# Performance work log

Measured on AMD Instinct MI355X. Metric: run time of the kernel, lower is better.

The kernel has to match this reference:

```python
import jax, jax.numpy as jnp
import numpy as np

D_MODEL = 1024
NUM_HEADS = 16
D_HEAD = D_MODEL // NUM_HEADS  # 64
LAMBDA_INIT = 0.8
EPS = 1e-5


def setup_inputs() -> dict:
    key = jax.random.key(0)
    ks = jax.random.split(key, 10)
    B, N = 2, 2048
    # Xavier-uniform-ish scale for the projection weights
    def xav(k, shape):
        fan_in, fan_out = shape[0], shape[1]
        lim = np.sqrt(6.0 / (fan_in + fan_out))
        return jax.random.uniform(k, shape, jnp.float32, -lim, lim)
    return {
        "X": jax.random.normal(ks[0], (B, N, D_MODEL), jnp.float32),
        "Wq": xav(ks[1], (D_MODEL, 2 * D_MODEL)),
        "Wk": xav(ks[2], (D_MODEL, 2 * D_MODEL)),
        "Wv": xav(ks[3], (D_MODEL, 2 * D_MODEL)),
        "Wo": xav(ks[4], (2 * D_MODEL, D_MODEL)),
        "lambda_q1": jax.random.normal(ks[5], (NUM_HEADS, D_HEAD), jnp.float32),
        "lambda_k1": jax.random.normal(ks[6], (NUM_HEADS, D_HEAD), jnp.float32),
        "lambda_q2": jax.random.normal(ks[7], (NUM_HEADS, D_HEAD), jnp.float32),
        "lambda_k2": jax.random.normal(ks[8], (NUM_HEADS, D_HEAD), jnp.float32),
        "rms_scale": jnp.ones((2 * D_HEAD,), jnp.float32),
    }


def reference(X, Wq, Wk, Wv, Wo, lambda_q1, lambda_k1, lambda_q2, lambda_k2, rms_scale):
    B, N, _ = X.shape
    H, Dh = NUM_HEADS, D_HEAD
    # projections -> [B, H, N, 2*Dh]
    Q = (X @ Wq).reshape(B, N, H, 2 * Dh).transpose(0, 2, 1, 3)
    K = (X @ Wk).reshape(B, N, H, 2 * Dh).transpose(0, 2, 1, 3)
    V = (X @ Wv).reshape(B, N, H, 2 * Dh).transpose(0, 2, 1, 3)
    Q1, Q2 = Q[..., :Dh], Q[..., Dh:]
    K1, K2 = K[..., :Dh], K[..., Dh:]
    # learned lambda per head
    lam = (jnp.exp(jnp.sum(lambda_q1 * lambda_k1, -1))
           - jnp.exp(jnp.sum(lambda_q2 * lambda_k2, -1))
           + LAMBDA_INIT)  # [H]
    scaling = 1.0 / np.sqrt(Dh)
    causal = jnp.tril(jnp.ones((N, N), bool))  # [N, N]
    neg_inf = jnp.float32(-jnp.inf)
    A1 = jnp.einsum('bhqd,bhkd->bhqk', Q1, K1) * scaling
    A2 = jnp.einsum('bhqd,bhkd->bhqk', Q2, K2) * scaling
    A1 = jnp.where(causal, A1, neg_inf)
    A2 = jnp.where(causal, A2, neg_inf)
    attn = jax.nn.softmax(A1, axis=-1) - lam[None, :, None, None] * jax.nn.softmax(A2, axis=-1)
    O = jnp.einsum('bhqk,bhkd->bhqd', attn, V)  # [B, H, N, 2*Dh]
    # per-(batch,head,pos) RMSNorm over the 2*Dh channel dim
    rms = jnp.sqrt(jnp.mean(O * O, axis=-1, keepdims=True) + EPS)
    O = O / rms * rms_scale
    O = O * (1.0 - LAMBDA_INIT)
    O = O.transpose(0, 2, 1, 3).reshape(B, N, H * 2 * Dh)
    return O @ Wo
```

## Files before the change

### kernel.cpp

```cpp
#include <hip/hip_runtime.h>
#include <hip/hip_bf16.h>

#define DM   1024
#define NH   16
#define DH   64
#define NSEQ 2048
#define NBATCH 2
#define ROWS (NBATCH*NSEQ)
#define QKVN (2*DM)
#define STR3 (3*DM*2)

typedef __attribute__((ext_vector_type(8))) short short8;
typedef __attribute__((ext_vector_type(4))) float f32x4;
typedef __attribute__((ext_vector_type(4))) unsigned short u16x4;

__device__ __forceinline__ unsigned short f2bf(float x) {
  union { float f; unsigned u; } v; v.f = x;
  unsigned r = v.u + 0x7FFFu + ((v.u >> 16) & 1u);
  return (unsigned short)(r >> 16);
}

__device__ __forceinline__ f32x4 mfma16(short8 a, short8 b, f32x4 c) {
  return __builtin_amdgcn_mfma_f32_16x16x32_bf16(a, b, c, 0, 0, 0);
}

#define GLL(src, dst) \
  __builtin_amdgcn_global_load_lds((const __attribute__((address_space(1))) void*)(src), \
                                   (__attribute__((address_space(3))) void*)(dst), 16, 0, 0)

__global__ void cast_f32_bf16(const float* __restrict__ in, unsigned short* __restrict__ out, int n4) {
  int i = blockIdx.x * blockDim.x + threadIdx.x;
  if (i >= n4) return;
  f32x4 v = *(const f32x4*)(in + (size_t)i * 4);
  u16x4 o;
  #pragma unroll
  for (int j = 0; j < 4; ++j) o[j] = f2bf(v[j]);
  *(u16x4*)(out + (size_t)i * 4) = o;
}

__global__ void transpose_cast_w(const float* __restrict__ in, unsigned short* __restrict__ out,
                                 int R, int C) {
  __shared__ float tile[32][33];
  const int bx = blockIdx.x, by = blockIdx.y;
  const int tx = threadIdx.x, ty = threadIdx.y;
  #pragma unroll
  for (int i = 0; i < 4; ++i)
    tile[ty + i*8][tx] = in[(size_t)(by*32 + ty + i*8) * C + bx*32 + tx];
  __syncthreads();
  #pragma unroll
  for (int i = 0; i < 4; ++i)
    out[(size_t)(bx*32 + ty + i*8) * R + by*32 + tx] = f2bf(tile[tx][ty + i*8]);
}

__global__ void transpose_v(const unsigned short* __restrict__ Vb, unsigned short* __restrict__ Vt) {
  __shared__ unsigned short tile[32][33];
  const int bx = blockIdx.x, by = blockIdx.y;
  const int tx = threadIdx.x, ty = threadIdx.y;
  #pragma unroll
  for (int i = 0; i < 4; ++i)
    tile[ty + i*8][tx] = Vb[(size_t)(by*32 + ty + i*8) * STR3 + bx*32 + tx];
  __syncthreads();
  #pragma unroll
  for (int i = 0; i < 4; ++i) {
    int colg = bx*32 + ty + i*8;
    int rowg = by*32 + tx;
    int hh = colg >> 7, dd = colg & 127;
    int bb = rowg >> 11, nn = rowg & 2047;
    Vt[(size_t)((bb*NH + hh)*128 + dd) * NSEQ + nn] = tile[tx][ty + i*8];
  }
}

__global__ void lam_kernel(const float* __restrict__ lq1, const float* __restrict__ lk1,
                           const float* __restrict__ lq2, const float* __restrict__ lk2,
                           float* __restrict__ lam) {
  int h = threadIdx.x >> 6, lane = threadIdx.x & 63;
  float p1 = lq1[h*64 + lane] * lk1[h*64 + lane];
  float p2 = lq2[h*64 + lane] * lk2[h*64 + lane];
  #pragma unroll
  for (int mk = 32; mk >= 1; mk >>= 1) {
    p1 += __shfl_xor(p1, mk);
    p2 += __shfl_xor(p2, mk);
  }
  if (lane == 0) lam[h] = expf(p1) - expf(p2) + 0.8f;
}

template <typename OT>
__global__ __launch_bounds__(256) void gemm_bt(const unsigned short* __restrict__ A,
                                               const unsigned short* __restrict__ Bt,
                                               OT* __restrict__ C, int M, int N, int K) {
  __shared__ __align__(16) unsigned short As[128*32];
  __shared__ __align__(16) unsigned short Bs[128*32];
  const int tid = threadIdx.x;
  const int w = tid >> 6, lane = tid & 63;
  const int l15 = lane & 15, lg = lane >> 4;
  const int wr = w >> 1, wc = w & 1;
  const int m0 = blockIdx.y * 128, n0 = blockIdx.x * 128;

  f32x4 acc[4][4];
  #pragma unroll
  for (int i = 0; i < 4; ++i)
    #pragma unroll
    for (int j = 0; j < 4; ++j) acc[i][j] = f32x4{0.f, 0.f, 0.f, 0.f};

  for (int kt = 0; kt < K; kt += 32) {
    #pragma unroll
    for (int j = 0; j < 2; ++j) {
      int cbase = (j*4 + w) * 64;
      int c = cbase + lane;
      const unsigned short* ga = A + (size_t)(m0 + (c >> 2)) * K + kt + (c & 3) * 8;
      GLL(ga, As + cbase*8);
      const unsigned short* gb = Bt + (size_t)(n0 + (c >> 2)) * K + kt + (c & 3) * 8;
      GLL(gb, Bs + cbase*8);
    }
    __syncthreads();
    short8 af[4], bfr[4];
    #pragma unroll
    for (int m = 0; m < 4; ++m)
      af[m] = *(const short8*)(As + (wr*64 + m*16 + l15) * 32 + lg*8);
    #pragma unroll
    for (int n = 0; n < 4; ++n)
      bfr[n] = *(const short8*)(Bs + (wc*64 + n*16 + l15) * 32 + lg*8);
    #pragma unroll
    for (int m = 0; m < 4; ++m)
      #pragma unroll
      for (int n = 0; n < 4; ++n)
        acc[m][n] = mfma16(af[m], bfr[n], acc[m][n]);
    __syncthreads();
  }

  #pragma unroll
  for (int m = 0; m < 4; ++m)
    #pragma unroll
    for (int n = 0; n < 4; ++n)
      #pragma unroll
      for (int r = 0; r < 4; ++r) {
        int row = m0 + wr*64 + m*16 + lg*4 + r;
        int col = n0 + wc*64 + n*16 + l15;
        if constexpr (sizeof(OT) == 2)
          C[(size_t)row * N + col] = f2bf(acc[m][n][r]);
        else
          C[(size_t)row * N + col] = acc[m][n][r];
      }
}

__global__ __launch_bounds__(256) void diff_attn(const unsigned short* __restrict__ QKV,
                                                 const unsigned short* __restrict__ Vt,
                                                 const float* __restrict__ lam_arr,
                                                 const float* __restrict__ rms_scale,
                                                 unsigned short* __restrict__ O) {
  __shared__ __align__(16) unsigned short Ks[2][64*128];
  __shared__ __align__(16) unsigned short Vs[2][128*64];
  __shared__ __align__(16) unsigned short Plds[4][2][16*64];
  const int bh = blockIdx.x;
  const int b = bh >> 4, h = bh & 15;
  const int w = threadIdx.x >> 6, lane = threadIdx.x & 63;
  const int l15 = lane & 15, lg = lane >> 4;
  const int yy = gridDim.y - 1 - blockIdx.y;
  const int q0 = yy * 64 + w * 16;
  const float lam = lam_arr[h];

  const unsigned short* Qb  = QKV + (size_t)(b * NSEQ) * STR3 + h * 128;
  const unsigned short* Kb  = QKV + (size_t)(b * NSEQ) * STR3 + 2048 + h * 128;
  const unsigned short* Vtb = Vt + (size_t)bh * 128 * NSEQ;

  short8 a1[2], a2[2];
  #pragma unroll
  for (int kc = 0; kc < 2; ++kc) {
    const unsigned short* qp = Qb + (size_t)(q0 + l15) * STR3 + kc*32 + lg*8;
    a1[kc] = *(const short8*)qp;
    a2[kc] = *(const short8*)(qp + 64);
  }

  auto stage = [&](int bufi, int key0) {
    #pragma unroll
    for (int j = 0; j < 4; ++j) {
      const int t = j*4 + w;
      {
        const int row = t*4 + (lane >> 4);
        const int ck  = lane & 15;
        const int cks = (ck & 8) | ((ck ^ row) & 7);
        GLL(Kb + (size_t)(key0 + row) * STR3 + cks*8, &Ks[bufi][t*512]);
      }
      {
        const int row = t*8 + (lane >> 3);
        const int ck  = lane & 7;
        const int cks = (ck ^ row) & 7;
        GLL(Vtb + (size_t)row * NSEQ + key0 + cks*8, &Vs[bufi][t*512]);
      }
    }
  };

  f32x4 o1[8], o2[8];
  #pragma unroll
  for (int i = 0; i < 8; ++i) { o1[i] = f32x4{0,0,0,0}; o2[i] = f32x4{0,0,0,0}; }
  float m1 = -3e38f, l1 = 0.f, m2 = -3e38f, l2 = 0.f;

  char* pb0 = (char*)&Plds[w][0][0];
  char* pb1 = (char*)&Plds[w][1][0];
  const unsigned swz = (unsigned)((l15 & 7) << 4);

  stage(0, 0);
  __syncthreads();
  int buf = 0;

  for (int kb = 0; kb <= yy; ++kb) {
    const int key0 = kb * 64;
    if (kb < yy) stage(buf ^ 1, key0 + 64);

    f32x4 st1[4], st2[4];
    #pragma unroll
    for (int nb = 0; nb < 4; ++nb) { st1[nb] = f32x4{0,0,0,0}; st2[nb] = f32x4{0,0,0,0}; }
    __builtin_amdgcn_s_setprio(1);
    #pragma unroll
    for (int nb = 0; nb < 4; ++nb) {
      const int row = nb*16 + l15;
      #pragma unroll
      for (int kc = 0; kc < 2; ++kc) {
        const unsigned short* kp = &Ks[buf][row*128 + (((kc*4 + lg) ^ row) & 7) * 8];
        short8 bk1 = *(const short8*)kp;
        short8 bk2 = *(const short8*)(kp + 64);
        st1[nb] = mfma16(bk1, a1[kc], st1[nb]);
        st2[nb] = mfma16(bk2, a2[kc], st2[nb]);
      }
    }
    __builtin_amdgcn_s_setprio(0);

    const bool need_mask = (key0 + 63 > q0);
    float tm1 = -3e38f, tm2 = -3e38f;
    #pragma unroll
    for (int nb = 0; nb < 4; ++nb)
      #pragma unroll
      for (int r = 0; r < 4; ++r) {
        float v1 = st1[nb][r] * 0.125f;
        float v2 = st2[nb][r] * 0.125f;
        if (need_mask && (key0 + nb*16 + lg*4 + r > q0 + l15)) { v1 = -3e38f; v2 = -3e38f; }
        st1[nb][r] = v1; st2[nb][r] = v2;
        tm1 = fmaxf(tm1, v1); tm2 = fmaxf(tm2, v2);
      }
    tm1 = fmaxf(tm1, __shfl_xor(tm1, 16));
    tm1 = fmaxf(tm1, __shfl_xor(tm1, 32));
    tm2 = fmaxf(tm2, __shfl_xor(tm2, 16));
    tm2 = fmaxf(tm2, __shfl_xor(tm2, 32));

    if (__any(tm1 > m1 + 8.f)) {
      const float nm = fmaxf(m1, tm1);
      const float e = __expf(m1 - nm);
      m1 = nm; l1 *= e;
      float er[4];
      #pragma unroll
      for (int r = 0; r < 4; ++r) er[r] = __shfl(e, lg*4 + r);
      #pragma unroll
      for (int i = 0; i < 8; ++i)
        #pragma unroll
        for (int r = 0; r < 4; ++r) o1[i][r] *= er[r];
    }
    if (__any(tm2 > m2 + 8.f)) {
      const float nm = fmaxf(m2, tm2);
      const float e = __expf(m2 - nm);
      m2 = nm; l2 *= e;
      float er[4];
      #pragma unroll
      for (int r = 0; r < 4; ++r) er[r] = __shfl(e, lg*4 + r);
      #pragma unroll
      for (int i = 0; i < 8; ++i)
        #pragma unroll
        for (int r = 0; r < 4; ++r) o2[i][r] *= er[r];
    }

    float ts1 = 0.f, ts2 = 0.f;
    #pragma unroll
    for (int nb = 0; nb < 4; ++nb)
      #pragma unroll
      for (int r = 0; r < 4; ++r) {
        st1[nb][r] = __expf(st1[nb][r] - m1); ts1 += st1[nb][r];
        st2[nb][r] = __expf(st2[nb][r] - m2); ts2 += st2[nb][r];
      }
    ts1 += __shfl_xor(ts1, 16); ts1 += __shfl_xor(ts1, 32); l1 += ts1;
    ts2 += __shfl_xor(ts2, 16); ts2 += __shfl_xor(ts2, 32); l2 += ts2;

    #pragma unroll
    for (int nb = 0; nb < 4; ++nb) {
      u16x4 k1, k2;
      #pragma unroll
      for (int r = 0; r < 4; ++r) { k1[r] = f2bf(st1[nb][r]); k2[r] = f2bf(st2[nb][r]); }
      const unsigned off = (unsigned)(l15*128 + nb*32 + lg*8) ^ swz;
      *(u16x4*)(pb0 + off) = k1;
      *(u16x4*)(pb1 + off) = k2;
    }
    asm volatile("s_waitcnt lgkmcnt(0)" ::: "memory");
    __builtin_amdgcn_sched_barrier(0);
    short8 pa1[2], pa2[2];
    #pragma unroll
    for (int kc = 0; kc < 2; ++kc) {
      const unsigned off = (unsigned)(l15*128 + kc*64 + lg*16) ^ swz;
      pa1[kc] = *(const short8*)(pb0 + off);
      pa2[kc] = *(const short8*)(pb1 + off);
    }
    __builtin_amdgcn_sched_barrier(0);

    __builtin_amdgcn_s_setprio(1);
    #pragma unroll
    for (int i = 0; i < 8; ++i) {
      const int row = i*16 + l15;
      #pragma unroll
      for (int kc = 0; kc < 2; ++kc) {
        const short8 bv = *(const short8*)(&Vs[buf][row*64 + (((kc*4 + lg) ^ row) & 7) * 8]);
        o1[i] = mfma16(pa1[kc], bv, o1[i]);
        o2[i] = mfma16(pa2[kc], bv, o2[i]);
      }
    }
    __builtin_amdgcn_s_setprio(0);

    __syncthreads();
    buf ^= 1;
  }

  float i1r[4], i2r[4];
  {
    const float inv1 = 1.f / l1, inv2 = 1.f / l2;
    #pragma unroll
    for (int r = 0; r < 4; ++r) {
      i1r[r] = __shfl(inv1, lg*4 + r);
      i2r[r] = __shfl(inv2, lg*4 + r);
    }
  }
  float ov[8][4];
  float ssq[4] = {0.f, 0.f, 0.f, 0.f};
  #pragma unroll
  for (int i = 0; i < 8; ++i)
    #pragma unroll
    for (int r = 0; r < 4; ++r) {
      float v = o1[i][r] * i1r[r] - lam * (o2[i][r] * i2r[r]);
      ov[i][r] = v;
      ssq[r] += v * v;
    }
  #pragma unroll
  for (int r = 0; r < 4; ++r)
    #pragma unroll
    for (int mk = 1; mk < 16; mk <<= 1) ssq[r] += __shfl_xor(ssq[r], mk);
  float rr[4];
  #pragma unroll
  for (int r = 0; r < 4; ++r) rr[r] = rsqrtf(ssq[r] * (1.f/128.f) + 1e-5f) * 0.2f;
  #pragma unroll
  for (int i = 0; i < 8; ++i) {
    const float sc = rms_scale[i*16 + l15];
    #pragma unroll
    for (int r = 0; r < 4; ++r) {
      const int q = q0 + lg*4 + r;
      O[(size_t)(b*NSEQ + q) * QKVN + h*128 + i*16 + l15] = f2bf(ov[i][r] * rr[r] * sc);
    }
  }
}

extern "C" void kernel_launch(void* const* d_in, const int* in_sizes, int n_in,
                              void* d_out, int out_size, void* d_ws, size_t ws_size,
                              hipStream_t stream) {
  (void)in_sizes; (void)n_in; (void)out_size; (void)ws_size;
  const float* X   = (const float*)d_in[0];
  const float* Wq  = (const float*)d_in[1];
  const float* Wk  = (const float*)d_in[2];
  const float* Wv  = (const float*)d_in[3];
  const float* Wo  = (const float*)d_in[4];
  const float* lq1 = (const float*)d_in[5];
  const float* lk1 = (const float*)d_in[6];
  const float* lq2 = (const float*)d_in[7];
  const float* lk2 = (const float*)d_in[8];
  const float* rs  = (const float*)d_in[9];
  float* out = (float*)d_out;

  char* ws = (char*)d_ws;
  const size_t MB = 1ull << 20;
  unsigned short* Xb  = (unsigned short*)(ws);
  unsigned short* Wt  = (unsigned short*)(ws + 8*MB);
  unsigned short* Wot = (unsigned short*)(ws + 20*MB);
  unsigned short* QKV = (unsigned short*)(ws + 24*MB);
  unsigned short* Ob  = (unsigned short*)(ws + 72*MB);
  float*          lamp = (float*)(ws + 88*MB);
  unsigned short* Vt  = (unsigned short*)(ws);

  cast_f32_bf16<<<(ROWS*DM/4 + 255)/256, 256, 0, stream>>>(X, Xb, ROWS*DM/4);
  transpose_cast_w<<<dim3(QKVN/32, DM/32), dim3(32,8), 0, stream>>>(Wq, Wt,             DM, QKVN);
  transpose_cast_w<<<dim3(QKVN/32, DM/32), dim3(32,8), 0, stream>>>(Wk, Wt + 2048*1024, DM, QKVN);
  transpose_cast_w<<<dim3(QKVN/32, DM/32), dim3(32,8), 0, stream>>>(Wv, Wt + 4096*1024, DM, QKVN);
  transpose_cast_w<<<dim3(DM/32, QKVN/32), dim3(32,8), 0, stream>>>(Wo, Wot, QKVN, DM);
  lam_kernel<<<1, 1024, 0, stream>>>(lq1, lk1, lq2, lk2, lamp);

  gemm_bt<unsigned short><<<dim3(STR3/128, ROWS/128), 256, 0, stream>>>(Xb, Wt, QKV, ROWS, STR3, DM);

  transpose_v<<<dim3(QKVN/32, ROWS/32), dim3(32,8), 0, stream>>>(QKV + 4096, Vt);

  diff_attn<<<dim3(NBATCH*NH, NSEQ/64), 256, 0, stream>>>(QKV, Vt, lamp, rs, Ob);

  gemm_bt<float><<<dim3(DM/128, ROWS/128), 256, 0, stream>>>(Ob, Wot, out, ROWS, DM, QKVN);
}
```

Measured before the change: 253.5 us.

## Remap blocks for XCD locality, fold softmax scale into Q, use native exp2/bf16 cvt

Adds an XCD-aware block index remap to both the GEMM and attention kernels so that blocks sharing data land on the same chiplet L2. The attention kernel also folds the 1/sqrt(d)·log2(e) scale into Q once at load time, uses v_exp_f32 (exp2) directly, and packs bf16 with v_cvt_pk_bf16_f32. It applies the causal mask only on the diagonal block. Together these cut per-iteration VALU work and L2 misses. The remap drops the reversed q-block order that scheduled heavy causal tiles first, and rounding Q after scaling changes numerics slightly.

```diff
diff --git a/kernel.cpp b/kernel.cpp
--- a/kernel.cpp
+++ b/kernel.cpp
@@ -18,6 +18,13 @@
   union { float f; unsigned u; } v; v.f = x;
   unsigned r = v.u + 0x7FFFu + ((v.u >> 16) & 1u);
   return (unsigned short)(r >> 16);
+}
+
+__device__ __forceinline__ float exp2a(float x) {
+  float r; asm("v_exp_f32 %0, %1" : "=v"(r) : "v"(x)); return r;
+}
+__device__ __forceinline__ unsigned cvtpk(float lo, float hi) {
+  unsigned d; asm("v_cvt_pk_bf16_f32 %0, %1, %2" : "=v"(d) : "v"(lo), "v"(hi)); return d;
 }
 
 __device__ __forceinline__ f32x4 mfma16(short8 a, short8 b, f32x4 c) {
@@ -94,7 +101,12 @@
   const int w = tid >> 6, lane = tid & 63;
   const int l15 = lane & 15, lg = lane >> 4;
   const int wr = w >> 1, wc = w & 1;
-  const int m0 = blockIdx.y * 128, n0 = blockIdx.x * 128;
+
+  const unsigned gx = gridDim.x;
+  unsigned bid = blockIdx.y * gx + blockIdx.x;
+  const unsigned cpx = (gx * gridDim.y) >> 3;
+  bid = (bid & 7u) * cpx + (bid >> 3);
+  const int m0 = (int)(bid / gx) * 128, n0 = (int)(bid % gx) * 128;
 
   f32x4 acc[4][4];
   #pragma unroll
@@ -151,11 +163,15 @@
   __shared__ __align__(16) unsigned short Ks[2][64*128];
   __shared__ __align__(16) unsigned short Vs[2][128*64];
   __shared__ __align__(16) unsigned short Plds[4][2][16*64];
-  const int bh = blockIdx.x;
+
+  unsigned bid = blockIdx.y * 32u + blockIdx.x;
+  const unsigned tile = (bid & 7u) * 128u + (bid >> 3);
+  const int bh = (int)(tile >> 5);
+  const int yy = (int)(tile & 31u);
+
   const int b = bh >> 4, h = bh & 15;
   const int w = threadIdx.x >> 6, lane = threadIdx.x & 63;
   const int l15 = lane & 15, lg = lane >> 4;
-  const int yy = gridDim.y - 1 - blockIdx.y;
   const int q0 = yy * 64 + w * 16;
   const float lam = lam_arr[h];
 
@@ -163,12 +179,27 @@
   const unsigned short* Kb  = QKV + (size_t)(b * NSEQ) * STR3 + 2048 + h * 128;
   const unsigned short* Vtb = Vt + (size_t)bh * 128 * NSEQ;
 
+  const float qsc = 0.125f * 1.44269504088896340736f;
   short8 a1[2], a2[2];
   #pragma unroll
   for (int kc = 0; kc < 2; ++kc) {
     const unsigned short* qp = Qb + (size_t)(q0 + l15) * STR3 + kc*32 + lg*8;
-    a1[kc] = *(const short8*)qp;
-    a2[kc] = *(const short8*)(qp + 64);
+    short8 r1 = *(const short8*)qp;
+    short8 r2 = *(const short8*)(qp + 64);
+    #pragma unroll
+    for (int j = 0; j < 8; j += 2) {
+      union { unsigned u; float f; } x0, x1, y0, y1;
+      x0.u = ((unsigned)(unsigned short)r1[j]) << 16;
+      x1.u = ((unsigned)(unsigned short)r1[j+1]) << 16;
+      y0.u = ((unsigned)(unsigned short)r2[j]) << 16;
+      y1.u = ((unsigned)(unsigned short)r2[j+1]) << 16;
+      unsigned d1 = cvtpk(x0.f * qsc, x1.f * qsc);
+      unsigned d2 = cvtpk(y0.f * qsc, y1.f * qsc);
+      a1[kc][j]   = (short)(unsigned short)(d1 & 0xffffu);
+      a1[kc][j+1] = (short)(unsigned short)(d1 >> 16);
+      a2[kc][j]   = (short)(unsigned short)(d2 & 0xffffu);
+      a2[kc][j+1] = (short)(unsigned short)(d2 >> 16);
+    }
   }
 
   auto stage = [&](int bufi, int key0) {
@@ -225,17 +256,20 @@
     }
     __builtin_amdgcn_s_setprio(0);
 
-    const bool need_mask = (key0 + 63 > q0);
+    if (kb == yy) {
+      #pragma unroll
+      for (int nb = 0; nb < 4; ++nb)
+        #pragma unroll
+        for (int r = 0; r < 4; ++r)
+          if (key0 + nb*16 + lg*4 + r > q0 + l15) { st1[nb][r] = -3e38f; st2[nb][r] = -3e38f; }
+    }
+
     float tm1 = -3e38f, tm2 = -3e38f;
     #pragma unroll
     for (int nb = 0; nb < 4; ++nb)
       #pragma unroll
       for (int r = 0; r < 4; ++r) {
-        float v1 = st1[nb][r] * 0.125f;
-        float v2 = st2[nb][r] * 0.125f;
-        if (need_mask && (key0 + nb*16 + lg*4 + r > q0 + l15)) { v1 = -3e38f; v2 = -3e38f; }
-        st1[nb][r] = v1; st2[nb][r] = v2;
-        tm1 = fmaxf(tm1, v1); tm2 = fmaxf(tm2, v2);
+        tm1 = fmaxf(tm1, st1[nb][r]); tm2 = fmaxf(tm2, st2[nb][r]);
       }
     tm1 = fmaxf(tm1, __shfl_xor(tm1, 16));
     tm1 = fmaxf(tm1, __shfl_xor(tm1, 32));
@@ -244,7 +278,7 @@
 
     if (__any(tm1 > m1 + 8.f)) {
       const float nm = fmaxf(m1, tm1);
-      const float e = __expf(m1 - nm);
+      const float e = exp2a(m1 - nm);
       m1 = nm; l1 *= e;
       float er[4];
       #pragma unroll
@@ -256,7 +290,7 @@
     }
     if (__any(tm2 > m2 + 8.f)) {
       const float nm = fmaxf(m2, tm2);
-      const float e = __expf(m2 - nm);
+      const float e = exp2a(m2 - nm);
       m2 = nm; l2 *= e;
       float er[4];
       #pragma unroll
@@ -272,20 +306,19 @@
     for (int nb = 0; nb < 4; ++nb)
       #pragma unroll
       for (int r = 0; r < 4; ++r) {
-        st1[nb][r] = __expf(st1[nb][r] - m1); ts1 += st1[nb][r];
-        st2[nb][r] = __expf(st2[nb][r] - m2); ts2 += st2[nb][r];
+        st1[nb][r] = exp2a(st1[nb][r] - m1); ts1 += st1[nb][r];
+        st2[nb][r] = exp2a(st2[nb][r] - m2); ts2 += st2[nb][r];
       }
     ts1 += __shfl_xor(ts1, 16); ts1 += __shfl_xor(ts1, 32); l1 += ts1;
     ts2 += __shfl_xor(ts2, 16); ts2 += __shfl_xor(ts2, 32); l2 += ts2;
 
     #pragma unroll
     for (int nb = 0; nb < 4; ++nb) {
-      u16x4 k1, k2;
-      #pragma unroll
-      for (int r = 0; r < 4; ++r) { k1[r] = f2bf(st1[nb][r]); k2[r] = f2bf(st2[nb][r]); }
       const unsigned off = (unsigned)(l15*128 + nb*32 + lg*8) ^ swz;
-      *(u16x4*)(pb0 + off) = k1;
-      *(u16x4*)(pb1 + off) = k2;
+      *(uint2*)(pb0 + off) = make_uint2(cvtpk(st1[nb][0], st1[nb][1]),
+                                        cvtpk(st1[nb][2], st1[nb][3]));
+      *(uint2*)(pb1 + off) = make_uint2(cvtpk(st2[nb][0], st2[nb][1]),
+                                        cvtpk(st2[nb][2], st2[nb][3]));
     }
     asm volatile("s_waitcnt lgkmcnt(0)" ::: "memory");
     __builtin_amdgcn_sched_barrier(0);
@@ -389,7 +422,7 @@
 
   transpose_v<<<dim3(QKVN/32, ROWS/32), dim3(32,8), 0, stream>>>(QKV + 4096, Vt);
 
-  diff_attn<<<dim3(NBATCH*NH, NSEQ/64), 256, 0, stream>>>(QKV, Vt, lamp, rs, Ob);
+  diff_attn<<<dim3(32, 32), 256, 0, stream>>>(QKV, Vt, lamp, rs, Ob);
 
   gemm_bt<float><<<dim3(DM/128, ROWS/128), 256, 0, stream>>>(Ob, Wot, out, ROWS, DM, QKVN);
 }
```

Result: slower. 293.7 us (+15.8%).
